# Kernel optimization log

Hardware: AMD Instinct MI355X
Metric: run time of the kernel (lower is better)

The kernel has to match this reference:

```python
import jax, jax.numpy as jnp
import numpy as np


def _conv(x, w, stride=1, pad=0):
    return jax.lax.conv_general_dilated(
        x, w, window_strides=(stride, stride),
        padding=[(pad, pad), (pad, pad)],
        dimension_numbers=('NCHW', 'OIHW', 'NCHW'))


def _frozen_bn(x, gamma, beta, mean, var):
    # FrozenBatchNorm2d: scale = gamma * rsqrt(var); bias = beta - mean*scale
    scale = gamma * jax.lax.rsqrt(var)
    bias = beta - mean * scale
    return x * scale[None, :, None, None] + bias[None, :, None, None]


def setup_inputs() -> dict:
    key = jax.random.key(0)
    ks = jax.random.split(key, 16)
    N, Cin, H, W = 32, 1024, 28, 28
    Cb, Cout = 256, 1024
    x = jax.random.normal(ks[0], (N, Cin, H, W), dtype=jnp.float32)
    # conv weights, kaiming-uniform-ish scale
    w1 = jax.random.uniform(ks[1], (Cb, Cin, 1, 1), minval=-1, maxval=1) * (1.0 / np.sqrt(Cin))
    w2 = jax.random.uniform(ks[2], (Cb, Cb, 3, 3), minval=-1, maxval=1) * (1.0 / np.sqrt(Cb * 9))
    w3 = jax.random.uniform(ks[3], (Cout, Cb, 1, 1), minval=-1, maxval=1) * (1.0 / np.sqrt(Cb))
    def bn_params(k, n):
        k1, k2, k3, k4 = jax.random.split(k, 4)
        gamma = jax.random.uniform(k1, (n,), minval=0.5, maxval=1.5)
        beta = jax.random.normal(k2, (n,)) * 0.1
        mean = jax.random.normal(k3, (n,)) * 0.1
        var = jax.random.uniform(k4, (n,), minval=0.5, maxval=1.5)
        return gamma, beta, mean, var
    g1, b1, m1, v1 = bn_params(ks[4], Cb)
    g2, b2, m2, v2 = bn_params(ks[5], Cb)
    g3, b3, m3, v3 = bn_params(ks[6], Cout)
    return dict(x=x, w1=w1, w2=w2, w3=w3,
                g1=g1, b1=b1, m1=m1, v1=v1,
                g2=g2, b2=b2, m2=m2, v2=v2,
                g3=g3, b3=b3, m3=m3, v3=v3)


def reference(x, w1, w2, w3, g1, b1, m1, v1, g2, b2, m2, v2, g3, b3, m3, v3):
    identity = x
    out = _conv(x, w1, stride=1, pad=0)          # 1x1: Cin -> Cb
    out = jax.nn.relu(_frozen_bn(out, g1, b1, m1, v1))
    out = _conv(out, w2, stride=1, pad=1)        # 3x3: Cb -> Cb
    out = jax.nn.relu(_frozen_bn(out, g2, b2, m2, v2))
    out = _conv(out, w3, stride=1, pad=0)        # 1x1: Cb -> Cout
    out = _frozen_bn(out, g3, b3, m3, v3)
    # stride==1 and in_channels==out_channels -> downsample is None
    out = jax.nn.relu(out + identity)
    return out
```

## Files before the change

kernel.cpp:

```cpp
#include <hip/hip_runtime.h>


#define BM 128
#define BNT 128
#define BK 64

typedef __attribute__((ext_vector_type(8))) short short8;
typedef __attribute__((ext_vector_type(4))) float f32x4;

__device__ inline unsigned short f2bf(float f) {
    unsigned int u = __float_as_uint(f);
    u += 0x7fff + ((u >> 16) & 1);
    return (unsigned short)(u >> 16);
}

__device__ inline void gload16(const unsigned short* g, unsigned short* l) {
    __builtin_amdgcn_global_load_lds(
        (const __attribute__((address_space(1))) unsigned int*)g,
        (__attribute__((address_space(3))) unsigned int*)l, 16, 0, 0);
}

__global__ __launch_bounds__(256) void prep_x(const float* __restrict__ x,
                                              unsigned short* __restrict__ Xh) {
    __shared__ float t[32][33];
    const int p0 = blockIdx.x * 32, c0 = blockIdx.y * 32, n = blockIdx.z;
    const int tid = threadIdx.x;
    const int pl = tid & 31, cl = tid >> 5;
    const float* xb = x + ((size_t)n * 1024 + c0) * 784;
    #pragma unroll
    for (int j = 0; j < 4; ++j) {
        int ci = cl + j * 8;
        int p = p0 + pl;
        t[ci][pl] = (p < 784) ? xb[(size_t)ci * 784 + p] : 0.f;
    }
    __syncthreads();
    const int c2 = (tid & 15) * 2, pr = tid >> 4;
    #pragma unroll
    for (int j = 0; j < 2; ++j) {
        int p = p0 + pr + j * 16;
        if (p < 784) {
            unsigned int pk = (unsigned)f2bf(t[c2][pr + j * 16]) |
                              ((unsigned)f2bf(t[c2 + 1][pr + j * 16]) << 16);
            *(unsigned int*)(Xh + (size_t)(n * 784 + p) * 1024 + c0 + c2) = pk;
        }
    }
}

__global__ __launch_bounds__(256) void prep_w(
    const float* __restrict__ w1, const float* __restrict__ w2, const float* __restrict__ w3,
    const float* g1, const float* b1, const float* m1, const float* v1,
    const float* g2, const float* b2, const float* m2, const float* v2,
    const float* g3, const float* b3, const float* m3, const float* v3,
    unsigned short* __restrict__ Wb1, unsigned short* __restrict__ Wt2,
    unsigned short* __restrict__ Wb3,
    float* __restrict__ bn1, float* __restrict__ bn2, float* __restrict__ bn3) {
    int i = blockIdx.x * 256 + threadIdx.x;
    if (i < 262144) Wb1[i] = f2bf(w1[i]);
    if (i < 589824) {
        int kw = i % 3, t1 = i / 3;
        int kh = t1 % 3, t2 = t1 / 3;
        int ci = t2 & 255, co = t2 >> 8;
        Wt2[(size_t)((kh * 3 + kw) * 256 + co) * 256 + ci] = f2bf(w2[i]);
    }
    if (i < 262144) Wb3[i] = f2bf(w3[i]);
    if (i < 256) { float s = g1[i] * rsqrtf(v1[i]); bn1[i] = s; bn1[256 + i] = b1[i] - m1[i] * s; }
    if (i < 256) { float s = g2[i] * rsqrtf(v2[i]); bn2[i] = s; bn2[256 + i] = b2[i] - m2[i] * s; }
    if (i < 1024) { float s = g3[i] * rsqrtf(v3[i]); bn3[i] = s; bn3[1024 + i] = b3[i] - m3[i] * s; }
}

__global__ __launch_bounds__(256) void zero16(uint4* __restrict__ p, int n) {
    int i = blockIdx.x * 256 + threadIdx.x;
    if (i < n) p[i] = make_uint4(0u, 0u, 0u, 0u);
}

template <int CX, int NTAPS, int LAYER>
__device__ __forceinline__ void conv_body(
    const unsigned short* __restrict__ Xg, const unsigned short* __restrict__ Wg,
    const float* __restrict__ bn, int nco,
    const float* __restrict__ residual,
    unsigned short* __restrict__ obf, float* __restrict__ ofp) {
    __shared__ __align__(16) char smem[LAYER == 3 ? 33792 : 32768];
    unsigned short* Xs = (unsigned short*)smem;
    unsigned short* Ws = (unsigned short*)(smem + 16384);
    const int tid = threadIdx.x;
    const int wave = tid >> 6, lane = tid & 63;
    const int quad = lane >> 4, l15 = lane & 15;
    const int Pb = blockIdx.x * BM;
    const int cb = blockIdx.y * BNT;
    const int wco = (wave & 1) * 64;
    const int wpx = (wave >> 1) * 64;

    int rowt[4], cso[4];
    size_t xrow[4];
    #pragma unroll
    for (int t = 0; t < 4; ++t) {
        int slot = t * 256 + tid;
        int row = slot >> 3;
        int c = slot & 7;
        rowt[t] = row;
        cso[t] = ((c ^ (row & 7)) * 8);
        if (LAYER == 2) {
            int P = Pb + row;
            int n = P / 784, rem = P - n * 784;
            int h = rem / 28, w = rem - h * 28;
            xrow[t] = (size_t)n * 900 + h * 30 + w;
        } else {
            xrow[t] = (size_t)(Pb + row);
        }
    }

    f32x4 acc[4][4];
    #pragma unroll
    for (int i = 0; i < 4; ++i)
        #pragma unroll
        for (int j = 0; j < 4; ++j)
            acc[i][j] = (f32x4){0.f, 0.f, 0.f, 0.f};

    for (int tap = 0; tap < NTAPS; ++tap) {
        const int tapofs = (NTAPS == 9) ? ((tap / 3) * 30 + (tap % 3)) : 0;
        const unsigned short* Wtap = Wg + (size_t)tap * 256 * CX;
        for (int k0 = 0; k0 < CX; k0 += BK) {
            __syncthreads();
            #pragma unroll
            for (int t = 0; t < 4; ++t) {
                unsigned short* xl = Xs + (size_t)(t * 256 + wave * 64) * 8;
                unsigned short* wl = Ws + (size_t)(t * 256 + wave * 64) * 8;
                const unsigned short* gx = Xg + (xrow[t] + tapofs) * (size_t)CX + k0 + cso[t];
                const unsigned short* gw = Wtap + (size_t)(cb + rowt[t]) * CX + k0 + cso[t];
                gload16(gx, xl);
                gload16(gw, wl);
            }
            __syncthreads();
            #pragma unroll
            for (int kk = 0; kk < BK; kk += 32) {
                short8 af[4], bf[4];
                const int cbase = kk >> 3;
                #pragma unroll
                for (int wi = 0; wi < 4; ++wi) {
                    int row = wco + wi * 16 + l15;
                    int ch = (cbase + quad) ^ (row & 7);
                    af[wi] = *(const short8*)(Ws + (row * 8 + ch) * 8);
                }
                #pragma unroll
                for (int wj = 0; wj < 4; ++wj) {
                    int row = wpx + wj * 16 + l15;
                    int ch = (cbase + quad) ^ (row & 7);
                    bf[wj] = *(const short8*)(Xs + (row * 8 + ch) * 8);
                }
                #pragma unroll
                for (int wi = 0; wi < 4; ++wi)
                    #pragma unroll
                    for (int wj = 0; wj < 4; ++wj)
                        acc[wi][wj] = __builtin_amdgcn_mfma_f32_16x16x32_bf16(
                            af[wi], bf[wj], acc[wi][wj], 0, 0, 0);
            }
        }
    }

    __syncthreads();

    if (LAYER == 3) {
        float* ep = (float*)smem;
        #pragma unroll
        for (int pass = 0; pass < 2; ++pass) {
            if ((wave & 1) == pass) {
                #pragma unroll
                for (int wi = 0; wi < 4; ++wi) {
                    int co0 = cb + wco + wi * 16 + quad * 4;
                    f32x4 sc = *(const f32x4*)(bn + co0);
                    f32x4 bi = *(const f32x4*)(bn + nco + co0);
                    int cr0 = wi * 16 + quad * 4;
                    #pragma unroll
                    for (int wj = 0; wj < 4; ++wj) {
                        int px = wpx + wj * 16 + l15;
                        #pragma unroll
                        for (int r = 0; r < 4; ++r)
                            ep[(cr0 + r) * 132 + px] = fmaf(acc[wi][wj][r], sc[r], bi[r]);
                    }
                }
            }
            __syncthreads();
            {
                int cr = tid >> 2;
                int cg = tid & 3;
                int co = cb + pass * 64 + cr;
                #pragma unroll
                for (int k = 0; k < 8; ++k) {
                    int px4 = (cg + 4 * k) * 4;
                    f32x4 v = *(const f32x4*)(ep + cr * 132 + px4);
                    int P = Pb + px4;
                    int n = P / 784, p = P - n * 784;
                    size_t off = ((size_t)n * 1024 + co) * 784 + p;
                    float4 rs = *(const float4*)(residual + off);
                    float4 o;
                    o.x = v[0] + rs.x; o.x = o.x > 0.f ? o.x : 0.f;
                    o.y = v[1] + rs.y; o.y = o.y > 0.f ? o.y : 0.f;
                    o.z = v[2] + rs.z; o.z = o.z > 0.f ? o.z : 0.f;
                    o.w = v[3] + rs.w; o.w = o.w > 0.f ? o.w : 0.f;
                    *(float4*)(ofp + off) = o;
                }
            }
            __syncthreads();
        }
    } else {
        unsigned short* ep = (unsigned short*)smem;
        #pragma unroll
        for (int pass = 0; pass < 2; ++pass) {
            if ((wave >> 1) == pass) {
                #pragma unroll
                for (int wi = 0; wi < 4; ++wi) {
                    int co0 = cb + wco + wi * 16 + quad * 4;
                    f32x4 sc = *(const f32x4*)(bn + co0);
                    f32x4 bi = *(const f32x4*)(bn + nco + co0);
                    int col = wco + wi * 16 + quad * 4;
                    #pragma unroll
                    for (int wj = 0; wj < 4; ++wj) {
                        int pxl = wj * 16 + l15;
                        float v0 = fmaf(acc[wi][wj][0], sc[0], bi[0]); v0 = v0 > 0.f ? v0 : 0.f;
                        float v1 = fmaf(acc[wi][wj][1], sc[1], bi[1]); v1 = v1 > 0.f ? v1 : 0.f;
                        float v2 = fmaf(acc[wi][wj][2], sc[2], bi[2]); v2 = v2 > 0.f ? v2 : 0.f;
                        float v3 = fmaf(acc[wi][wj][3], sc[3], bi[3]); v3 = v3 > 0.f ? v3 : 0.f;
                        uint2 pk;
                        pk.x = (unsigned)f2bf(v0) | ((unsigned)f2bf(v1) << 16);
                        pk.y = (unsigned)f2bf(v2) | ((unsigned)f2bf(v3) << 16);
                        *(uint2*)(ep + pxl * 136 + col) = pk;
                    }
                }
            }
            __syncthreads();
            {
                int pxl = tid >> 2;
                int cg = tid & 3;
                int P = Pb + pass * 64 + pxl;
                size_t orow;
                if (LAYER == 1) {
                    int n = P / 784, rem = P - n * 784;
                    int h = rem / 28, w = rem - h * 28;
                    orow = (size_t)n * 900 + (h + 1) * 30 + (w + 1);
                } else {
                    orow = (size_t)P;
                }
                #pragma unroll
                for (int k = 0; k < 4; ++k) {
                    int cc = (cg + 4 * k) * 8;
                    uint4 v = *(const uint4*)(ep + pxl * 136 + cc);
                    *(uint4*)(obf + orow * 256 + cb + cc) = v;
                }
            }
            __syncthreads();
        }
    }
}

__global__ __launch_bounds__(256) void conv1_mfma(
    const unsigned short* __restrict__ Xg, const unsigned short* __restrict__ Wg,
    const float* __restrict__ bn, unsigned short* __restrict__ obf) {
    conv_body<1024, 1, 1>(Xg, Wg, bn, 256, nullptr, obf, nullptr);
}
__global__ __launch_bounds__(256) void conv2_mfma(
    const unsigned short* __restrict__ Xg, const unsigned short* __restrict__ Wg,
    const float* __restrict__ bn, unsigned short* __restrict__ obf) {
    conv_body<256, 9, 2>(Xg, Wg, bn, 256, nullptr, obf, nullptr);
}
__global__ __launch_bounds__(256) void conv3_mfma(
    const unsigned short* __restrict__ Xg, const unsigned short* __restrict__ Wg,
    const float* __restrict__ bn, const float* __restrict__ residual,
    float* __restrict__ ofp) {
    conv_body<256, 1, 3>(Xg, Wg, bn, 1024, residual, nullptr, ofp);
}

extern "C" void kernel_launch(void* const* d_in, const int* in_sizes, int n_in,
                              void* d_out, int out_size, void* d_ws, size_t ws_size,
                              hipStream_t stream) {
    const float* x  = (const float*)d_in[0];
    const float* w1 = (const float*)d_in[1];
    const float* w2 = (const float*)d_in[2];
    const float* w3 = (const float*)d_in[3];
    const float* g1 = (const float*)d_in[4];  const float* b1 = (const float*)d_in[5];
    const float* m1 = (const float*)d_in[6];  const float* v1 = (const float*)d_in[7];
    const float* g2 = (const float*)d_in[8];  const float* b2 = (const float*)d_in[9];
    const float* m2 = (const float*)d_in[10]; const float* v2 = (const float*)d_in[11];
    const float* g3 = (const float*)d_in[12]; const float* b3 = (const float*)d_in[13];
    const float* m3 = (const float*)d_in[14]; const float* v3 = (const float*)d_in[15];
    float* out = (float*)d_out;

    char* ws = (char*)d_ws;
    unsigned short* Xh  = (unsigned short*)(ws);
    unsigned short* y1p = (unsigned short*)(ws + 51380224);
    unsigned short* y2  = (unsigned short*)(ws + 66125824);
    unsigned short* Wb1 = (unsigned short*)(ws + 78970880);
    unsigned short* Wt2 = (unsigned short*)(ws + 79495168);
    unsigned short* Wb3 = (unsigned short*)(ws + 80674816);
    float* bn1 = (float*)(ws + 81199104);
    float* bn2 = (float*)(ws + 81201152);
    float* bn3 = (float*)(ws + 81203200);

    prep_x<<<dim3(25, 32, 32), 256, 0, stream>>>(x, Xh);
    prep_w<<<2304, 256, 0, stream>>>(w1, w2, w3,
                                     g1, b1, m1, v1, g2, b2, m2, v2, g3, b3, m3, v3,
                                     Wb1, Wt2, Wb3, bn1, bn2, bn3);
    zero16<<<3600, 256, 0, stream>>>((uint4*)y1p, 921600);

    conv1_mfma<<<dim3(196, 2), 256, 0, stream>>>(Xh, Wb1, bn1, y1p);
    conv2_mfma<<<dim3(196, 2), 256, 0, stream>>>(y1p, Wt2, bn2, y2);
    conv3_mfma<<<dim3(196, 8), 256, 0, stream>>>(y2, Wb3, bn3, x, out);
}
```

Before: 343.2 us.

## Double-buffer conv1/conv2 LDS staging, vectorize x transpose, zero only padding border

Conv1 and conv2 now use two LDS buffers and prefetch the next K-slice with global_load_lds while the current one runs through MFMA, leaving one barrier per iteration instead of two. The x NCHW-to-NHWC bf16 transpose moves to 64x64 tiles with float4 loads and 16-byte stores. The full clear of the padded y1 buffer is replaced by a kernel that writes zeros only to the one-pixel border. Doubling LDS to 64KB per block may lower occupancy. The prep_x float4 guard assumes 784 is divisible by 4, which holds.

```diff
diff --git a/kernel.cpp b/kernel.cpp
--- a/kernel.cpp
+++ b/kernel.cpp
@@ -22,26 +22,41 @@
 
 __global__ __launch_bounds__(256) void prep_x(const float* __restrict__ x,
                                               unsigned short* __restrict__ Xh) {
-    __shared__ float t[32][33];
-    const int p0 = blockIdx.x * 32, c0 = blockIdx.y * 32, n = blockIdx.z;
+    __shared__ float t[64 * 65];
+    const int p0 = blockIdx.x * 64, c0 = blockIdx.y * 64, n = blockIdx.z;
     const int tid = threadIdx.x;
-    const int pl = tid & 31, cl = tid >> 5;
-    const float* xb = x + ((size_t)n * 1024 + c0) * 784;
-    #pragma unroll
-    for (int j = 0; j < 4; ++j) {
-        int ci = cl + j * 8;
-        int p = p0 + pl;
-        t[ci][pl] = (p < 784) ? xb[(size_t)ci * 784 + p] : 0.f;
+    {
+        const int px4 = (tid & 15) * 4;
+        const int r0 = tid >> 4;
+        const float* xb = x + ((size_t)n * 1024 + c0 + r0) * 784 + p0 + px4;
+        #pragma unroll
+        for (int j = 0; j < 4; ++j) {
+            int row = r0 + j * 16;
+            float4 v = make_float4(0.f, 0.f, 0.f, 0.f);
+            if (p0 + px4 + 3 < 784) v = *(const float4*)(xb + (size_t)j * 16 * 784);
+            t[row * 65 + px4 + 0] = v.x;
+            t[row * 65 + px4 + 1] = v.y;
+            t[row * 65 + px4 + 2] = v.z;
+            t[row * 65 + px4 + 3] = v.w;
+        }
     }
     __syncthreads();
-    const int c2 = (tid & 15) * 2, pr = tid >> 4;
-    #pragma unroll
-    for (int j = 0; j < 2; ++j) {
-        int p = p0 + pr + j * 16;
-        if (p < 784) {
-            unsigned int pk = (unsigned)f2bf(t[c2][pr + j * 16]) |
-                              ((unsigned)f2bf(t[c2 + 1][pr + j * 16]) << 16);
-            *(unsigned int*)(Xh + (size_t)(n * 784 + p) * 1024 + c0 + c2) = pk;
+    {
+        const int cg = tid & 7;
+        #pragma unroll
+        for (int r2 = 0; r2 < 2; ++r2) {
+            int px = (tid >> 3) + 32 * r2;
+            if (p0 + px < 784) {
+                unsigned pk[4];
+                #pragma unroll
+                for (int j = 0; j < 4; ++j) {
+                    float f0 = t[(cg * 8 + 2 * j) * 65 + px];
+                    float f1 = t[(cg * 8 + 2 * j + 1) * 65 + px];
+                    pk[j] = (unsigned)f2bf(f0) | ((unsigned)f2bf(f1) << 16);
+                }
+                *(uint4*)(Xh + (size_t)(n * 784 + p0 + px) * 1024 + c0 + cg * 8) =
+                    make_uint4(pk[0], pk[1], pk[2], pk[3]);
+            }
         }
     }
 }
@@ -68,20 +83,29 @@
     if (i < 1024) { float s = g3[i] * rsqrtf(v3[i]); bn3[i] = s; bn3[1024 + i] = b3[i] - m3[i] * s; }
 }
 
-__global__ __launch_bounds__(256) void zero16(uint4* __restrict__ p, int n) {
+__global__ __launch_bounds__(256) void border_zero(uint4* __restrict__ y1p) {
     int i = blockIdx.x * 256 + threadIdx.x;
-    if (i < n) p[i] = make_uint4(0u, 0u, 0u, 0u);
-}
-
-template <int CX, int NTAPS, int LAYER>
+    int ch8 = i & 31;
+    int t = i >> 5;
+    int cell = t % 116;
+    int n = t / 116;
+    int h, w;
+    if (cell < 30)      { h = 0;          w = cell; }
+    else if (cell < 60) { h = 29;         w = cell - 30; }
+    else if (cell < 88) { h = cell - 59;  w = 0; }
+    else                { h = cell - 87;  w = 29; }
+    y1p[((size_t)n * 900 + h * 30 + w) * 32 + ch8] = make_uint4(0u, 0u, 0u, 0u);
+}
+
+template <int CX, int NTAPS, int LAYER, int DBUF>
 __device__ __forceinline__ void conv_body(
     const unsigned short* __restrict__ Xg, const unsigned short* __restrict__ Wg,
     const float* __restrict__ bn, int nco,
     const float* __restrict__ residual,
     unsigned short* __restrict__ obf, float* __restrict__ ofp) {
-    __shared__ __align__(16) char smem[LAYER == 3 ? 33792 : 32768];
-    unsigned short* Xs = (unsigned short*)smem;
-    unsigned short* Ws = (unsigned short*)(smem + 16384);
+    constexpr int KITER = CX / BK;
+    constexpr int NIT = NTAPS * KITER;
+    __shared__ __align__(16) char smem[DBUF ? 65536 : (LAYER == 3 ? 33792 : 32768)];
     const int tid = threadIdx.x;
     const int wave = tid >> 6, lane = tid & 63;
     const int quad = lane >> 4, l15 = lane & 15;
@@ -116,44 +140,63 @@
         for (int j = 0; j < 4; ++j)
             acc[i][j] = (f32x4){0.f, 0.f, 0.f, 0.f};
 
-    for (int tap = 0; tap < NTAPS; ++tap) {
+    auto stage = [&](int it, int b) {
+        unsigned short* Xs = (unsigned short*)(smem + b * 32768);
+        unsigned short* Ws = (unsigned short*)(smem + b * 32768 + 16384);
+        const int tap = (NTAPS == 1) ? 0 : it / KITER;
+        const int k0 = (it % KITER) * BK;
         const int tapofs = (NTAPS == 9) ? ((tap / 3) * 30 + (tap % 3)) : 0;
         const unsigned short* Wtap = Wg + (size_t)tap * 256 * CX;
-        for (int k0 = 0; k0 < CX; k0 += BK) {
-            __syncthreads();
+        #pragma unroll
+        for (int t = 0; t < 4; ++t)
+            gload16(Wtap + (size_t)(cb + rowt[t]) * CX + k0 + cso[t],
+                    Ws + (size_t)(t * 256 + wave * 64) * 8);
+        #pragma unroll
+        for (int t = 0; t < 4; ++t)
+            gload16(Xg + (xrow[t] + tapofs) * (size_t)CX + k0 + cso[t],
+                    Xs + (size_t)(t * 256 + wave * 64) * 8);
+    };
+    auto compute = [&](int b) {
+        unsigned short* Xs = (unsigned short*)(smem + b * 32768);
+        unsigned short* Ws = (unsigned short*)(smem + b * 32768 + 16384);
+        #pragma unroll
+        for (int kk = 0; kk < BK; kk += 32) {
+            short8 af[4], bf[4];
+            const int cbase = kk >> 3;
             #pragma unroll
-            for (int t = 0; t < 4; ++t) {
-                unsigned short* xl = Xs + (size_t)(t * 256 + wave * 64) * 8;
-                unsigned short* wl = Ws + (size_t)(t * 256 + wave * 64) * 8;
-                const unsigned short* gx = Xg + (xrow[t] + tapofs) * (size_t)CX + k0 + cso[t];
-                const unsigned short* gw = Wtap + (size_t)(cb + rowt[t]) * CX + k0 + cso[t];
-                gload16(gx, xl);
-                gload16(gw, wl);
-            }
-            __syncthreads();
+            for (int wi = 0; wi < 4; ++wi) {
+                int row = wco + wi * 16 + l15;
+                int ch = (cbase + quad) ^ (row & 7);
+                af[wi] = *(const short8*)(Ws + (row * 8 + ch) * 8);
+            }
             #pragma unroll
-            for (int kk = 0; kk < BK; kk += 32) {
-                short8 af[4], bf[4];
-                const int cbase = kk >> 3;
-                #pragma unroll
-                for (int wi = 0; wi < 4; ++wi) {
-                    int row = wco + wi * 16 + l15;
-                    int ch = (cbase + quad) ^ (row & 7);
-                    af[wi] = *(const short8*)(Ws + (row * 8 + ch) * 8);
-                }
-                #pragma unroll
-                for (int wj = 0; wj < 4; ++wj) {
-                    int row = wpx + wj * 16 + l15;
-                    int ch = (cbase + quad) ^ (row & 7);
-                    bf[wj] = *(const short8*)(Xs + (row * 8 + ch) * 8);
-                }
-                #pragma unroll
-                for (int wi = 0; wi < 4; ++wi)
-                    #pragma unroll
-                    for (int wj = 0; wj < 4; ++wj)
-                        acc[wi][wj] = __builtin_amdgcn_mfma_f32_16x16x32_bf16(
-                            af[wi], bf[wj], acc[wi][wj], 0, 0, 0);
-            }
+            for (int wj = 0; wj < 4; ++wj) {
+                int row = wpx + wj * 16 + l15;
+                int ch = (cbase + quad) ^ (row & 7);
+                bf[wj] = *(const short8*)(Xs + (row * 8 + ch) * 8);
+            }
+            #pragma unroll
+            for (int wi = 0; wi < 4; ++wi)
+                #pragma unroll
+                for (int wj = 0; wj < 4; ++wj)
+                    acc[wi][wj] = __builtin_amdgcn_mfma_f32_16x16x32_bf16(
+                        af[wi], bf[wj], acc[wi][wj], 0, 0, 0);
+        }
+    };
+
+    if (DBUF) {
+        stage(0, 0);
+        for (int it = 0; it < NIT; ++it) {
+            __syncthreads();
+            if (it + 1 < NIT) stage(it + 1, (it + 1) & 1);
+            compute(it & 1);
+        }
+    } else {
+        for (int it = 0; it < NIT; ++it) {
+            __syncthreads();
+            stage(it, 0);
+            __syncthreads();
+            compute(0);
         }
     }
 
@@ -255,18 +298,18 @@
 __global__ __launch_bounds__(256) void conv1_mfma(
     const unsigned short* __restrict__ Xg, const unsigned short* __restrict__ Wg,
     const float* __restrict__ bn, unsigned short* __restrict__ obf) {
-    conv_body<1024, 1, 1>(Xg, Wg, bn, 256, nullptr, obf, nullptr);
+    conv_body<1024, 1, 1, 1>(Xg, Wg, bn, 256, nullptr, obf, nullptr);
 }
 __global__ __launch_bounds__(256) void conv2_mfma(
     const unsigned short* __restrict__ Xg, const unsigned short* __restrict__ Wg,
     const float* __restrict__ bn, unsigned short* __restrict__ obf) {
-    conv_body<256, 9, 2>(Xg, Wg, bn, 256, nullptr, obf, nullptr);
+    conv_body<256, 9, 2, 1>(Xg, Wg, bn, 256, nullptr, obf, nullptr);
 }
 __global__ __launch_bounds__(256) void conv3_mfma(
     const unsigned short* __restrict__ Xg, const unsigned short* __restrict__ Wg,
     const float* __restrict__ bn, const float* __restrict__ residual,
     float* __restrict__ ofp) {
-    conv_body<256, 1, 3>(Xg, Wg, bn, 1024, residual, nullptr, ofp);
+    conv_body<256, 1, 3, 0>(Xg, Wg, bn, 1024, residual, nullptr, ofp);
 }
 
 extern "C" void kernel_launch(void* const* d_in, const int* in_sizes, int n_in,
@@ -295,11 +338,11 @@
     float* bn2 = (float*)(ws + 81201152);
     float* bn3 = (float*)(ws + 81203200);
 
-    prep_x<<<dim3(25, 32, 32), 256, 0, stream>>>(x, Xh);
+    prep_x<<<dim3(13, 16, 32), 256, 0, stream>>>(x, Xh);
     prep_w<<<2304, 256, 0, stream>>>(w1, w2, w3,
                                      g1, b1, m1, v1, g2, b2, m2, v2, g3, b3, m3, v3,
                                      Wb1, Wt2, Wb3, bn1, bn2, bn3);
-    zero16<<<3600, 256, 0, stream>>>((uint4*)y1p, 921600);
+    border_zero<<<464, 256, 0, stream>>>((uint4*)y1p);
 
     conv1_mfma<<<dim3(196, 2), 256, 0, stream>>>(Xh, Wb1, bn1, y1p);
     conv2_mfma<<<dim3(196, 2), 256, 0, stream>>>(y1p, Wt2, bn2, y2);
```

Measured after the change: 332.2 us. -3.2%, faster.
